# Kernel tuning notes

Measured on AMD Instinct MI355X. Metric: run time of the kernel, lower is better.

## Reference

```python
import jax, jax.numpy as jnp
import numpy as np

N, NF, DIM, H, DH, DEPTH, EDIM, NB = 256, 127, 128, 8, 64, 6, 3, 512
INNER = H * DH  # 512
SCALE = DH ** -0.5
EPS = 1e-5


def setup_inputs() -> dict:
    key = jax.random.key(0)
    ks = jax.random.split(key, 16)
    p = lambda k, shape: jax.random.normal(k, shape, jnp.float32) * 0.02
    return {
        "coordinates": jax.random.normal(ks[0], (N, 3), jnp.float32),
        "bonds": jax.random.randint(ks[1], (NB, 2), 0, N),
        "noise_level": jax.random.uniform(ks[2], (1,), jnp.float32),
        "atom_emb": p(ks[3], (N, NF)),
        "ln1_g": jnp.ones((DEPTH, DIM)), "ln1_b": jnp.zeros((DEPTH, DIM)),
        "Wq": p(ks[4], (DEPTH, DIM, INNER)), "bq": jnp.zeros((DEPTH, INNER)),
        "Wkv": p(ks[5], (DEPTH, DIM, 2 * INNER)), "bkv": jnp.zeros((DEPTH, 2 * INNER)),
        "We": p(ks[6], (DEPTH, EDIM, INNER)), "be": jnp.zeros((DEPTH, INNER)),
        "Wo": p(ks[7], (DEPTH, INNER, DIM)), "bo": jnp.zeros((DEPTH, DIM)),
        "Wg1": p(ks[8], (DEPTH, 3 * DIM)),
        "ln2_g": jnp.ones((DEPTH, DIM)), "ln2_b": jnp.zeros((DEPTH, DIM)),
        "W1": p(ks[9], (DEPTH, DIM, 4 * DIM)), "b1": jnp.zeros((DEPTH, 4 * DIM)),
        "W2": p(ks[10], (DEPTH, 4 * DIM, DIM)), "b2": jnp.zeros((DEPTH, DIM)),
        "Wg2": p(ks[11], (DEPTH, 3 * DIM)),
        "out_w": p(ks[12], (DIM, 1)), "out_b": jnp.zeros((1,)),
    }


def _layernorm(x, g, b):
    m = jnp.mean(x, axis=-1, keepdims=True)
    v = jnp.mean((x - m) ** 2, axis=-1, keepdims=True)
    return (x - m) * jax.lax.rsqrt(v + EPS) * g + b


def _gated_residual(x, res, Wg):
    # Linear(3*dim -> 1, no bias) then sigmoid; mask is all-True so no masking.
    gate = jax.nn.sigmoid(jnp.concatenate([x, res, x - res], axis=-1) @ Wg)[..., None]
    return x * gate + res * (1.0 - gate)


def _forward(coordinates, bonds, noise_level, atom_emb, ln1_g, ln1_b, Wq, bq,
             Wkv, bkv, We, be, Wo, bo, Wg1, ln2_g, ln2_b, W1, b1, W2, b2, Wg2,
             out_w, out_b):
    n = coordinates.shape[0]
    # nodes: [n, NF] atom embeddings (looked up at arange(n)) + noise column -> [n, DIM]
    noise_col = jnp.broadcast_to(noise_level.reshape(1, 1), (n, 1))
    nodes = jnp.concatenate([atom_emb, noise_col], axis=-1)
    # dense edge tensor [n, n, 3]: coordinate differences at bonded pairs, antisymmetric
    bi, bj = bonds[:, 0], bonds[:, 1]
    diff = coordinates[bi] - coordinates[bj]
    edges = jnp.zeros((n, n, EDIM), jnp.float32).at[bi, bj].set(diff).at[bj, bi].set(-diff)

    for l in range(DEPTH):
        # --- edge-biased multi-head attention (PreNorm) ---
        x = _layernorm(nodes, ln1_g[l], ln1_b[l])
        q = (x @ Wq[l] + bq[l]).reshape(n, H, DH).transpose(1, 0, 2)          # [h, i, d]
        kv = x @ Wkv[l] + bkv[l]
        k = kv[:, :INNER].reshape(n, H, DH).transpose(1, 0, 2)                # [h, j, d]
        v = kv[:, INNER:].reshape(n, H, DH).transpose(1, 0, 2)                # [h, j, d]
        e = (edges @ We[l] + be[l]).reshape(n, n, H, DH).transpose(2, 0, 1, 3)  # [h, i, j, d]
        k_ij = k[:, None, :, :] + e                                            # [h, i, j, d]
        v_ij = v[:, None, :, :] + e
        sim = jnp.einsum('hid,hijd->hij', q, k_ij) * SCALE
        attn = jax.nn.softmax(sim, axis=-1)  # mask is all ones -> no-op
        out = jnp.einsum('hij,hijd->hid', attn, v_ij)                          # [h, i, d]
        out = out.transpose(1, 0, 2).reshape(n, INNER) @ Wo[l] + bo[l]         # [n, DIM]
        nodes = _gated_residual(out, nodes, Wg1[l])
        # --- feedforward (PreNorm) + gated residual ---
        y = _layernorm(nodes, ln2_g[l], ln2_b[l])
        y = jax.nn.gelu(y @ W1[l] + b1[l], approximate=False) @ W2[l] + b2[l]
        nodes = _gated_residual(y, nodes, Wg2[l])

    energy = nodes @ out_w + out_b  # [n, 1]
    return energy[None, :, :]       # [1, n, 1]


def reference(coordinates, bonds, noise_level, atom_emb, ln1_g, ln1_b, Wq, bq,
              Wkv, bkv, We, be, Wo, bo, Wg1, ln2_g, ln2_b, W1, b1, W2, b2, Wg2,
              out_w, out_b):
    return _forward(coordinates, bonds, noise_level, atom_emb, ln1_g, ln1_b,
                    Wq, bq, Wkv, bkv, We, be, Wo, bo, Wg1, ln2_g, ln2_b,
                    W1, b1, W2, b2, Wg2, out_w, out_b)
```

## Files before the change

### kernel.cpp

```cpp
#include <hip/hip_runtime.h>

#define NN     256
#define NF     127
#define DIM    128
#define NH     8
#define DH     64
#define INNER  512
#define DEPTH  6
#define NB     512
#define ATTN_SCALE 0.125f
#define LN_EPS 1e-5f

__device__ __forceinline__ float wred_sum(float v){
#pragma unroll
  for(int o=32;o;o>>=1) v += __shfl_xor(v,o);
  return v;
}
__device__ __forceinline__ float wred_max(float v){
#pragma unroll
  for(int o=32;o;o>>=1) v = fmaxf(v,__shfl_xor(v,o));
  return v;
}
__device__ __forceinline__ float block_sum(float v, float* sred, int t){
  v = wred_sum(v);
  __syncthreads();
  if((t&63)==0) sred[t>>6]=v;
  __syncthreads();
  float s = 0.f;
#pragma unroll
  for(int w=0; w<8; w++) s += sred[w];
  return s;
}

__device__ __forceinline__ void dev_ln(const float* in, float* out,
                                       const float* g, const float* b,
                                       float* sred, int t){
  float v = (t<DIM)? in[t] : 0.f;
  float m = block_sum(v,sred,t) * (1.f/DIM);
  float d = (t<DIM)? (v-m) : 0.f;
  float var = block_sum(d*d,sred,t) * (1.f/DIM);
  float rs = rsqrtf(var + LN_EPS);
  if(t<DIM) out[t] = d*rs*g[t] + b[t];
  __syncthreads();
}

__device__ __forceinline__ void dev_qkv4(const float* xs, int i,
    const float* Wq, const float* bq, const float* Wkv, const float* bkv,
    const float* be, float* qg, float* kT, float* vg, float* redS, int t){
  {
    const int cg4 = (t&127)*4, rq = t>>7;
    float4 acc = make_float4(0.f,0.f,0.f,0.f);
#pragma unroll
    for(int f=rq*32; f<rq*32+32; f++){
      float x = xs[f];
      float4 w = *(const float4*)(Wq + f*INNER + cg4);
      acc.x=fmaf(x,w.x,acc.x); acc.y=fmaf(x,w.y,acc.y);
      acc.z=fmaf(x,w.z,acc.z); acc.w=fmaf(x,w.w,acc.w);
    }
    *(float4*)(redS + rq*INNER + cg4) = acc;
  }
  __syncthreads();
  qg[i*INNER+t] = bq[t] + redS[t] + redS[INNER+t] + redS[2*INNER+t] + redS[3*INNER+t];
  __syncthreads();
  {
    const int cg4 = (t&255)*4, rh = t>>8;
    float4 acc = make_float4(0.f,0.f,0.f,0.f);
#pragma unroll 8
    for(int f=rh*64; f<rh*64+64; f++){
      float x = xs[f];
      float4 w = *(const float4*)(Wkv + f*(2*INNER) + cg4);
      acc.x=fmaf(x,w.x,acc.x); acc.y=fmaf(x,w.y,acc.y);
      acc.z=fmaf(x,w.z,acc.z); acc.w=fmaf(x,w.w,acc.w);
    }
    *(float4*)(redS + rh*(2*INNER) + cg4) = acc;
  }
  __syncthreads();
#pragma unroll
  for(int cc=0; cc<2; cc++){
    int c = t + cc*512;
    float s = redS[c] + redS[2*INNER+c] + bkv[c];
    if(c < INNER) kT[c*NN+i]          = s + be[c];
    else          vg[i*INNER+c-INNER] = s + be[c-INNER];
  }
  __syncthreads();
}

__global__ __launch_bounds__(512) void k_qkv0(const float* atom_emb, const float* noise,
    float* nodes,
    const float* ln1_g, const float* ln1_b,
    const float* Wq, const float* bq, const float* Wkv, const float* bkv, const float* be,
    float* qg, float* kT, float* vg){
  __shared__ float nd[DIM], xs[DIM], sred[8], redS[2048];
  int t = threadIdx.x, i = blockIdx.x;
  if(t<DIM){
    float v = (t<NF)? atom_emb[i*NF+t] : noise[0];
    nd[t] = v;
    nodes[i*DIM+t] = v;
  }
  __syncthreads();
  dev_ln(nd, xs, ln1_g, ln1_b, sred, t);
  dev_qkv4(xs, i, Wq, bq, Wkv, bkv, be, qg, kT, vg, redS, t);
}

__global__ __launch_bounds__(512) void k_layer(
    float* nodes, const float* qg, const float* kT, const float* vg,
    float* qg_n, float* kT_n, float* vg_n,
    const int* bonds, const float* coords,
    const float* We,
    const float* Wo, const float* bo, const float* Wg1,
    const float* ln2_g, const float* ln2_b,
    const float* W1, const float* b1, const float* W2, const float* b2,
    const float* Wg2,
    const float* ln1_g_n, const float* ln1_b_n,
    const float* Wq_n, const float* bq_n, const float* Wkv_n, const float* bkv_n,
    const float* be_n, int has_next)
{
  __shared__ float nd[DIM], xs[DIM], qs[INNER], ao[INNER], o128[DIM];
  __shared__ float eL[NN*3], aW[NH*NN], redS[2048], sred[8], qWe[NH*3];
  const int t = threadIdx.x, i = blockIdx.x;

  if(t<DIM) nd[t] = nodes[i*DIM+t];
  qs[t] = qg[i*INNER+t];
  eL[t] = 0.f;
  if(t<NN) eL[512+t] = 0.f;
  __syncthreads();

  {
    int bi = bonds[2*t], bj = bonds[2*t+1];
    if(bi==i || bj==i){
      float dx = coords[3*bi+0] - coords[3*bj+0];
      float dy = coords[3*bi+1] - coords[3*bj+1];
      float dz = coords[3*bi+2] - coords[3*bj+2];
      if(bi==i){ eL[bj*3+0]=dx;  eL[bj*3+1]=dy;  eL[bj*3+2]=dz;  }
      if(bj==i){ eL[bi*3+0]=-dx; eL[bi*3+1]=-dy; eL[bi*3+2]=-dz; }
    }
  }
  __syncthreads();

  if(t < NH*3){
    int h = t/3, c = t%3;
    float acc = 0.f;
    for(int d=0; d<DH; d++) acc = fmaf(qs[h*DH+d], We[c*INNER + h*DH + d], acc);
    qWe[t] = acc;
  }
  __syncthreads();

  {
    const int h = t>>6, l = t&63, j0 = 4*l;
    const float* kTh = kT + (h*DH)*NN;
    float s0=0.f,s1=0.f,s2=0.f,s3=0.f;
#pragma unroll 8
    for(int o=0; o<DH; o++){
      float qv = qs[h*DH+o];
      float4 kk = *(const float4*)(kTh + o*NN + j0);
      s0=fmaf(qv,kk.x,s0); s1=fmaf(qv,kk.y,s1); s2=fmaf(qv,kk.z,s2); s3=fmaf(qv,kk.w,s3);
    }
    float w0=qWe[h*3+0], w1=qWe[h*3+1], w2=qWe[h*3+2];
    s0 += w0*eL[(j0+0)*3+0] + w1*eL[(j0+0)*3+1] + w2*eL[(j0+0)*3+2];
    s1 += w0*eL[(j0+1)*3+0] + w1*eL[(j0+1)*3+1] + w2*eL[(j0+1)*3+2];
    s2 += w0*eL[(j0+2)*3+0] + w1*eL[(j0+2)*3+1] + w2*eL[(j0+2)*3+2];
    s3 += w0*eL[(j0+3)*3+0] + w1*eL[(j0+3)*3+1] + w2*eL[(j0+3)*3+2];
    s0*=ATTN_SCALE; s1*=ATTN_SCALE; s2*=ATTN_SCALE; s3*=ATTN_SCALE;
    float mx = wred_max(fmaxf(fmaxf(s0,s1),fmaxf(s2,s3)));
    float p0=expf(s0-mx), p1=expf(s1-mx), p2=expf(s2-mx), p3=expf(s3-mx);
    float inv = 1.f / wred_sum(p0+p1+p2+p3);
    float a0=p0*inv, a1=p1*inv, a2=p2*inv, a3=p3*inv;
    float* aw = aW + h*NN;
    *(float4*)(aw + j0) = make_float4(a0,a1,a2,a3);
    float c0 = a0*eL[(j0+0)*3+0]+a1*eL[(j0+1)*3+0]+a2*eL[(j0+2)*3+0]+a3*eL[(j0+3)*3+0];
    float c1 = a0*eL[(j0+0)*3+1]+a1*eL[(j0+1)*3+1]+a2*eL[(j0+2)*3+1]+a3*eL[(j0+3)*3+1];
    float c2 = a0*eL[(j0+0)*3+2]+a1*eL[(j0+1)*3+2]+a2*eL[(j0+2)*3+2]+a3*eL[(j0+3)*3+2];
    c0 = wred_sum(c0); c1 = wred_sum(c1); c2 = wred_sum(c2);
    __builtin_amdgcn_wave_barrier();
    const int dq = (l&15)*4, jg = l>>4;
    const float* vb = vg + h*DH + dq;
    float4 acc = make_float4(0.f,0.f,0.f,0.f);
#pragma unroll 8
    for(int jj=0; jj<64; jj++){
      int j = jg*64 + jj;
      float a = aw[j];
      float4 vv = *(const float4*)(vb + j*INNER);
      acc.x=fmaf(a,vv.x,acc.x); acc.y=fmaf(a,vv.y,acc.y);
      acc.z=fmaf(a,vv.z,acc.z); acc.w=fmaf(a,vv.w,acc.w);
    }
#pragma unroll
    for(int o=16;o<64;o<<=1){
      acc.x += __shfl_xor(acc.x,o); acc.y += __shfl_xor(acc.y,o);
      acc.z += __shfl_xor(acc.z,o); acc.w += __shfl_xor(acc.w,o);
    }
    if(l<16){
      float4 we0 = *(const float4*)(We + 0*INNER + h*DH + dq);
      float4 we1 = *(const float4*)(We + 1*INNER + h*DH + dq);
      float4 we2 = *(const float4*)(We + 2*INNER + h*DH + dq);
      float4 o;
      o.x = acc.x + c0*we0.x + c1*we1.x + c2*we2.x;
      o.y = acc.y + c0*we0.y + c1*we1.y + c2*we2.y;
      o.z = acc.z + c0*we0.z + c1*we1.z + c2*we2.z;
      o.w = acc.w + c0*we0.w + c1*we1.w + c2*we2.w;
      *(float4*)(ao + h*DH + dq) = o;
    }
  }
  __syncthreads();

  {
    const int cg4 = (t&31)*4, rg = t>>5;
    float4 acc = make_float4(0.f,0.f,0.f,0.f);
#pragma unroll
    for(int r=rg*32; r<rg*32+32; r++){
      float a = ao[r];
      float4 w = *(const float4*)(Wo + r*DIM + cg4);
      acc.x=fmaf(a,w.x,acc.x); acc.y=fmaf(a,w.y,acc.y);
      acc.z=fmaf(a,w.z,acc.z); acc.w=fmaf(a,w.w,acc.w);
    }
    *(float4*)(redS + rg*DIM + cg4) = acc;
    __syncthreads();
    if(t<DIM){
      float s = bo[t];
#pragma unroll
      for(int g=0; g<16; g++) s += redS[g*DIM+t];
      o128[t] = s;
    }
    __syncthreads();
    float gv = 0.f;
    if(t<DIM){
      float o = o128[t], r = nd[t];
      gv = o*Wg1[t] + r*Wg1[DIM+t] + (o-r)*Wg1[2*DIM+t];
    }
    float gs = block_sum(gv, sred, t);
    float gate = 1.f/(1.f + expf(-gs));
    if(t<DIM) nd[t] = o128[t]*gate + nd[t]*(1.f-gate);
    __syncthreads();
  }

  dev_ln(nd, xs, ln2_g, ln2_b, sred, t);
  {
    const int cg4 = (t&127)*4, rq = t>>7;
    float4 acc = make_float4(0.f,0.f,0.f,0.f);
#pragma unroll
    for(int f=rq*32; f<rq*32+32; f++){
      float x = xs[f];
      float4 w = *(const float4*)(W1 + f*INNER + cg4);
      acc.x=fmaf(x,w.x,acc.x); acc.y=fmaf(x,w.y,acc.y);
      acc.z=fmaf(x,w.z,acc.z); acc.w=fmaf(x,w.w,acc.w);
    }
    *(float4*)(redS + rq*INNER + cg4) = acc;
  }
  __syncthreads();
  {
    float a = b1[t] + redS[t] + redS[INNER+t] + redS[2*INNER+t] + redS[3*INNER+t];
    qs[t] = 0.5f*a*(1.f + erff(a*0.70710678118654752440f));
  }
  __syncthreads();
  {
    const int cg4 = (t&31)*4, rg = t>>5;
    float4 acc = make_float4(0.f,0.f,0.f,0.f);
#pragma unroll
    for(int m=rg*32; m<rg*32+32; m++){
      float a = qs[m];
      float4 w = *(const float4*)(W2 + m*DIM + cg4);
      acc.x=fmaf(a,w.x,acc.x); acc.y=fmaf(a,w.y,acc.y);
      acc.z=fmaf(a,w.z,acc.z); acc.w=fmaf(a,w.w,acc.w);
    }
    *(float4*)(redS + rg*DIM + cg4) = acc;
    __syncthreads();
    if(t<DIM){
      float s = b2[t];
#pragma unroll
      for(int g=0; g<16; g++) s += redS[g*DIM+t];
      o128[t] = s;
    }
    __syncthreads();
    float gv = 0.f;
    if(t<DIM){
      float y = o128[t], r = nd[t];
      gv = y*Wg2[t] + r*Wg2[DIM+t] + (y-r)*Wg2[2*DIM+t];
    }
    float gs = block_sum(gv, sred, t);
    float gate = 1.f/(1.f + expf(-gs));
    if(t<DIM) nd[t] = o128[t]*gate + nd[t]*(1.f-gate);
    __syncthreads();
  }
  if(t<DIM) nodes[i*DIM+t] = nd[t];

  if(has_next){
    dev_ln(nd, xs, ln1_g_n, ln1_b_n, sred, t);
    dev_qkv4(xs, i, Wq_n, bq_n, Wkv_n, bkv_n, be_n, qg_n, kT_n, vg_n, redS, t);
  }
}

__global__ __launch_bounds__(64) void k_energy(const float* nodes, const float* out_w,
                                               const float* out_b, float* out){
  int i = blockIdx.x, l = threadIdx.x;
  float a = fmaf(nodes[i*DIM+l], out_w[l], nodes[i*DIM+64+l]*out_w[64+l]);
  a = wred_sum(a);
  if(l==0) out[i] = a + out_b[0];
}

extern "C" void kernel_launch(void* const* d_in, const int* in_sizes, int n_in,
                              void* d_out, int out_size, void* d_ws, size_t ws_size,
                              hipStream_t stream){
  const float* coords   = (const float*)d_in[0];
  const int*   bonds    = (const int*  )d_in[1];
  const float* noise    = (const float*)d_in[2];
  const float* atom_emb = (const float*)d_in[3];
  const float* ln1_g = (const float*)d_in[4];
  const float* ln1_b = (const float*)d_in[5];
  const float* Wq    = (const float*)d_in[6];
  const float* bq    = (const float*)d_in[7];
  const float* Wkv   = (const float*)d_in[8];
  const float* bkv   = (const float*)d_in[9];
  const float* We    = (const float*)d_in[10];
  const float* be    = (const float*)d_in[11];
  const float* Wo    = (const float*)d_in[12];
  const float* bo    = (const float*)d_in[13];
  const float* Wg1   = (const float*)d_in[14];
  const float* ln2_g = (const float*)d_in[15];
  const float* ln2_b = (const float*)d_in[16];
  const float* W1    = (const float*)d_in[17];
  const float* b1    = (const float*)d_in[18];
  const float* W2    = (const float*)d_in[19];
  const float* b2    = (const float*)d_in[20];
  const float* Wg2   = (const float*)d_in[21];
  const float* out_w = (const float*)d_in[22];
  const float* out_b = (const float*)d_in[23];

  float* ws = (float*)d_ws;
  float* nodes   = ws;
  float* qbuf[2] = { ws +  32768, ws + 163840 };
  float* kbuf[2] = { ws + 294912, ws + 425984 };
  float* vbuf[2] = { ws + 557056, ws + 688128 };

  k_qkv0<<<256, 512, 0, stream>>>(atom_emb, noise, nodes, ln1_g, ln1_b,
                                  Wq, bq, Wkv, bkv, be,
                                  qbuf[0], kbuf[0], vbuf[0]);
  for(int l=0; l<DEPTH; l++){
    int cur = l&1, nxt = cur^1;
    int has_next = (l < DEPTH-1);
    int ln = has_next ? l+1 : l;
    k_layer<<<256, 512, 0, stream>>>(
      nodes, qbuf[cur], kbuf[cur], vbuf[cur],
      qbuf[nxt], kbuf[nxt], vbuf[nxt],
      bonds, coords,
      We  + (size_t)l*3*INNER,
      Wo  + (size_t)l*INNER*DIM, bo + (size_t)l*DIM, Wg1 + (size_t)l*3*DIM,
      ln2_g + (size_t)l*DIM, ln2_b + (size_t)l*DIM,
      W1  + (size_t)l*DIM*4*DIM, b1 + (size_t)l*4*DIM,
      W2  + (size_t)l*4*DIM*DIM, b2 + (size_t)l*DIM, Wg2 + (size_t)l*3*DIM,
      ln1_g + (size_t)ln*DIM, ln1_b + (size_t)ln*DIM,
      Wq  + (size_t)ln*DIM*INNER, bq + (size_t)ln*INNER,
      Wkv + (size_t)ln*DIM*2*INNER, bkv + (size_t)ln*2*INNER,
      be  + (size_t)ln*INNER, has_next);
  }
  k_energy<<<256, 64, 0, stream>>>(nodes, out_w, out_b, (float*)d_out);
}
```

Before: 320.1 us.

## Process two atoms per block to reuse weight and K/V loads

```diff
diff --git a/kernel.cpp b/kernel.cpp
--- a/kernel.cpp
+++ b/kernel.cpp
@@ -21,66 +21,97 @@
   for(int o=32;o;o>>=1) v = fmaxf(v,__shfl_xor(v,o));
   return v;
 }
-__device__ __forceinline__ float block_sum(float v, float* sred, int t){
-  v = wred_sum(v);
-  __syncthreads();
-  if((t&63)==0) sred[t>>6]=v;
-  __syncthreads();
-  float s = 0.f;
-#pragma unroll
-  for(int w=0; w<8; w++) s += sred[w];
-  return s;
-}
-
-__device__ __forceinline__ void dev_ln(const float* in, float* out,
-                                       const float* g, const float* b,
-                                       float* sred, int t){
-  float v = (t<DIM)? in[t] : 0.f;
-  float m = block_sum(v,sred,t) * (1.f/DIM);
-  float d = (t<DIM)? (v-m) : 0.f;
-  float var = block_sum(d*d,sred,t) * (1.f/DIM);
-  float rs = rsqrtf(var + LN_EPS);
-  if(t<DIM) out[t] = d*rs*g[t] + b[t];
-  __syncthreads();
-}
-
-__device__ __forceinline__ void dev_qkv4(const float* xs, int i,
+__device__ __forceinline__ float2 block_sum2(float v0, float v1, float* sred, int t){
+  v0 = wred_sum(v0); v1 = wred_sum(v1);
+  __syncthreads();
+  if((t&63)==0){ sred[t>>6]=v0; sred[8+(t>>6)]=v1; }
+  __syncthreads();
+  float s0=0.f, s1=0.f;
+#pragma unroll
+  for(int w=0; w<8; w++){ s0 += sred[w]; s1 += sred[8+w]; }
+  return make_float2(s0,s1);
+}
+
+__device__ __forceinline__ void dev_ln2(const float* in0, const float* in1,
+                                        float* out0, float* out1,
+                                        const float* g, const float* b,
+                                        float* sred, int t){
+  float v0 = (t<DIM)? in0[t] : 0.f;
+  float v1 = (t<DIM)? in1[t] : 0.f;
+  float2 m = block_sum2(v0,v1,sred,t);
+  float m0 = m.x*(1.f/DIM), m1 = m.y*(1.f/DIM);
+  float d0 = (t<DIM)? (v0-m0) : 0.f;
+  float d1 = (t<DIM)? (v1-m1) : 0.f;
+  float2 vv = block_sum2(d0*d0,d1*d1,sred,t);
+  float rs0 = rsqrtf(vv.x*(1.f/DIM) + LN_EPS);
+  float rs1 = rsqrtf(vv.y*(1.f/DIM) + LN_EPS);
+  if(t<DIM){
+    float gg = g[t], bb = b[t];
+    out0[t] = d0*rs0*gg + bb;
+    out1[t] = d1*rs1*gg + bb;
+  }
+  __syncthreads();
+}
+
+__device__ __forceinline__ void dev_qkv2(const float* xs0, const float* xs1, int i0,
     const float* Wq, const float* bq, const float* Wkv, const float* bkv,
-    const float* be, float* qg, float* kT, float* vg, float* redS, int t){
+    const float* be, float* qg, float* kT, float* vg, float* scratch, int t){
   {
     const int cg4 = (t&127)*4, rq = t>>7;
-    float4 acc = make_float4(0.f,0.f,0.f,0.f);
+    float4 a0 = make_float4(0.f,0.f,0.f,0.f);
+    float4 a1 = make_float4(0.f,0.f,0.f,0.f);
 #pragma unroll
     for(int f=rq*32; f<rq*32+32; f++){
-      float x = xs[f];
+      float x0 = xs0[f], x1 = xs1[f];
       float4 w = *(const float4*)(Wq + f*INNER + cg4);
-      acc.x=fmaf(x,w.x,acc.x); acc.y=fmaf(x,w.y,acc.y);
-      acc.z=fmaf(x,w.z,acc.z); acc.w=fmaf(x,w.w,acc.w);
-    }
-    *(float4*)(redS + rq*INNER + cg4) = acc;
-  }
-  __syncthreads();
-  qg[i*INNER+t] = bq[t] + redS[t] + redS[INNER+t] + redS[2*INNER+t] + redS[3*INNER+t];
+      a0.x=fmaf(x0,w.x,a0.x); a0.y=fmaf(x0,w.y,a0.y);
+      a0.z=fmaf(x0,w.z,a0.z); a0.w=fmaf(x0,w.w,a0.w);
+      a1.x=fmaf(x1,w.x,a1.x); a1.y=fmaf(x1,w.y,a1.y);
+      a1.z=fmaf(x1,w.z,a1.z); a1.w=fmaf(x1,w.w,a1.w);
+    }
+    *(float4*)(scratch + rq*INNER + cg4)        = a0;
+    *(float4*)(scratch + 2048 + rq*INNER + cg4) = a1;
+  }
+  __syncthreads();
+  {
+    float bqt = bq[t];
+    qg[i0*INNER+t]     = bqt + scratch[t] + scratch[INNER+t]
+                             + scratch[2*INNER+t] + scratch[3*INNER+t];
+    qg[(i0+1)*INNER+t] = bqt + scratch[2048+t] + scratch[2048+INNER+t]
+                             + scratch[2048+2*INNER+t] + scratch[2048+3*INNER+t];
+  }
   __syncthreads();
   {
     const int cg4 = (t&255)*4, rh = t>>8;
-    float4 acc = make_float4(0.f,0.f,0.f,0.f);
+    float4 a0 = make_float4(0.f,0.f,0.f,0.f);
+    float4 a1 = make_float4(0.f,0.f,0.f,0.f);
 #pragma unroll 8
     for(int f=rh*64; f<rh*64+64; f++){
-      float x = xs[f];
+      float x0 = xs0[f], x1 = xs1[f];
       float4 w = *(const float4*)(Wkv + f*(2*INNER) + cg4);
-      acc.x=fmaf(x,w.x,acc.x); acc.y=fmaf(x,w.y,acc.y);
-      acc.z=fmaf(x,w.z,acc.z); acc.w=fmaf(x,w.w,acc.w);
-    }
-    *(float4*)(redS + rh*(2*INNER) + cg4) = acc;
+      a0.x=fmaf(x0,w.x,a0.x); a0.y=fmaf(x0,w.y,a0.y);
+      a0.z=fmaf(x0,w.z,a0.z); a0.w=fmaf(x0,w.w,a0.w);
+      a1.x=fmaf(x1,w.x,a1.x); a1.y=fmaf(x1,w.y,a1.y);
+      a1.z=fmaf(x1,w.z,a1.z); a1.w=fmaf(x1,w.w,a1.w);
+    }
+    *(float4*)(scratch + rh*1024 + cg4)        = a0;
+    *(float4*)(scratch + 2048 + rh*1024 + cg4) = a1;
   }
   __syncthreads();
 #pragma unroll
   for(int cc=0; cc<2; cc++){
     int c = t + cc*512;
-    float s = redS[c] + redS[2*INNER+c] + bkv[c];
-    if(c < INNER) kT[c*NN+i]          = s + be[c];
-    else          vg[i*INNER+c-INNER] = s + be[c-INNER];
+    float bk = bkv[c];
+    float s0 = scratch[c]      + scratch[1024+c]      + bk;
+    float s1 = scratch[2048+c] + scratch[2048+1024+c] + bk;
+    if(c < INNER){
+      float bec = be[c];
+      *(float2*)(kT + c*NN + i0) = make_float2(s0+bec, s1+bec);
+    } else {
+      float bec = be[c-INNER];
+      vg[i0*INNER+c-INNER]     = s0 + bec;
+      vg[(i0+1)*INNER+c-INNER] = s1 + bec;
+    }
   }
   __syncthreads();
 }
@@ -90,16 +121,18 @@
     const float* ln1_g, const float* ln1_b,
     const float* Wq, const float* bq, const float* Wkv, const float* bkv, const float* be,
     float* qg, float* kT, float* vg){
-  __shared__ float nd[DIM], xs[DIM], sred[8], redS[2048];
-  int t = threadIdx.x, i = blockIdx.x;
+  __shared__ float nd0[DIM], nd1[DIM], xs0[DIM], xs1[DIM], sred[16], scratch[4096];
+  int t = threadIdx.x, i0 = blockIdx.x*2;
   if(t<DIM){
-    float v = (t<NF)? atom_emb[i*NF+t] : noise[0];
-    nd[t] = v;
-    nodes[i*DIM+t] = v;
-  }
-  __syncthreads();
-  dev_ln(nd, xs, ln1_g, ln1_b, sred, t);
-  dev_qkv4(xs, i, Wq, bq, Wkv, bkv, be, qg, kT, vg, redS, t);
+    float nz = noise[0];
+    float v0 = (t<NF)? atom_emb[i0*NF+t]     : nz;
+    float v1 = (t<NF)? atom_emb[(i0+1)*NF+t] : nz;
+    nd0[t]=v0; nd1[t]=v1;
+    nodes[i0*DIM+t]=v0; nodes[(i0+1)*DIM+t]=v1;
+  }
+  __syncthreads();
+  dev_ln2(nd0, nd1, xs0, xs1, ln1_g, ln1_b, sred, t);
+  dev_qkv2(xs0, xs1, i0, Wq, bq, Wkv, bkv, be, qg, kT, vg, scratch, t);
 }
 
 __global__ __launch_bounds__(512) void k_layer(
@@ -115,32 +148,39 @@
     const float* Wq_n, const float* bq_n, const float* Wkv_n, const float* bkv_n,
     const float* be_n, int has_next)
 {
-  __shared__ float nd[DIM], xs[DIM], qs[INNER], ao[INNER], o128[DIM];
-  __shared__ float eL[NN*3], aW[NH*NN], redS[2048], sred[8], qWe[NH*3];
-  const int t = threadIdx.x, i = blockIdx.x;
-
-  if(t<DIM) nd[t] = nodes[i*DIM+t];
-  qs[t] = qg[i*INNER+t];
-  eL[t] = 0.f;
-  if(t<NN) eL[512+t] = 0.f;
+  __shared__ float nd0[DIM], nd1[DIM], xs0[DIM], xs1[DIM];
+  __shared__ float qs0[INNER], qs1[INNER], ao0[INNER], ao1[INNER];
+  __shared__ float o1280[DIM], o1281[DIM];
+  __shared__ float eL0[NN*3], eL1[NN*3];
+  __shared__ float scratch[4096];
+  __shared__ float sred[16], qWe[2*NH*3];
+  const int t = threadIdx.x, i0 = blockIdx.x*2, i1 = i0+1;
+
+  if(t<DIM){ nd0[t] = nodes[i0*DIM+t]; nd1[t] = nodes[i1*DIM+t]; }
+  qs0[t] = qg[i0*INNER+t]; qs1[t] = qg[i1*INNER+t];
+  eL0[t] = 0.f; eL1[t] = 0.f;
+  if(t<NN){ eL0[512+t] = 0.f; eL1[512+t] = 0.f; }
   __syncthreads();
 
   {
     int bi = bonds[2*t], bj = bonds[2*t+1];
-    if(bi==i || bj==i){
+    if(bi==i0||bj==i0||bi==i1||bj==i1){
       float dx = coords[3*bi+0] - coords[3*bj+0];
       float dy = coords[3*bi+1] - coords[3*bj+1];
       float dz = coords[3*bi+2] - coords[3*bj+2];
-      if(bi==i){ eL[bj*3+0]=dx;  eL[bj*3+1]=dy;  eL[bj*3+2]=dz;  }
-      if(bj==i){ eL[bi*3+0]=-dx; eL[bi*3+1]=-dy; eL[bi*3+2]=-dz; }
-    }
-  }
-  __syncthreads();
-
-  if(t < NH*3){
-    int h = t/3, c = t%3;
+      if(bi==i0){ eL0[bj*3+0]=dx;  eL0[bj*3+1]=dy;  eL0[bj*3+2]=dz;  }
+      if(bj==i0){ eL0[bi*3+0]=-dx; eL0[bi*3+1]=-dy; eL0[bi*3+2]=-dz; }
+      if(bi==i1){ eL1[bj*3+0]=dx;  eL1[bj*3+1]=dy;  eL1[bj*3+2]=dz;  }
+      if(bj==i1){ eL1[bi*3+0]=-dx; eL1[bi*3+1]=-dy; eL1[bi*3+2]=-dz; }
+    }
+  }
+  __syncthreads();
+
+  if(t < 2*NH*3){
+    int r = t/24, rem = t%24, h = rem/3, c = rem%3;
+    const float* qsr = r? qs1 : qs0;
     float acc = 0.f;
-    for(int d=0; d<DH; d++) acc = fmaf(qs[h*DH+d], We[c*INNER + h*DH + d], acc);
+    for(int d=0; d<DH; d++) acc = fmaf(qsr[h*DH+d], We[c*INNER + h*DH + d], acc);
     qWe[t] = acc;
   }
   __syncthreads();
@@ -148,143 +188,208 @@
   {
     const int h = t>>6, l = t&63, j0 = 4*l;
     const float* kTh = kT + (h*DH)*NN;
-    float s0=0.f,s1=0.f,s2=0.f,s3=0.f;
+    float4 sA = make_float4(0.f,0.f,0.f,0.f);
+    float4 sB = make_float4(0.f,0.f,0.f,0.f);
 #pragma unroll 8
     for(int o=0; o<DH; o++){
-      float qv = qs[h*DH+o];
+      float qa = qs0[h*DH+o], qb = qs1[h*DH+o];
       float4 kk = *(const float4*)(kTh + o*NN + j0);
-      s0=fmaf(qv,kk.x,s0); s1=fmaf(qv,kk.y,s1); s2=fmaf(qv,kk.z,s2); s3=fmaf(qv,kk.w,s3);
-    }
-    float w0=qWe[h*3+0], w1=qWe[h*3+1], w2=qWe[h*3+2];
-    s0 += w0*eL[(j0+0)*3+0] + w1*eL[(j0+0)*3+1] + w2*eL[(j0+0)*3+2];
-    s1 += w0*eL[(j0+1)*3+0] + w1*eL[(j0+1)*3+1] + w2*eL[(j0+1)*3+2];
-    s2 += w0*eL[(j0+2)*3+0] + w1*eL[(j0+2)*3+1] + w2*eL[(j0+2)*3+2];
-    s3 += w0*eL[(j0+3)*3+0] + w1*eL[(j0+3)*3+1] + w2*eL[(j0+3)*3+2];
-    s0*=ATTN_SCALE; s1*=ATTN_SCALE; s2*=ATTN_SCALE; s3*=ATTN_SCALE;
-    float mx = wred_max(fmaxf(fmaxf(s0,s1),fmaxf(s2,s3)));
-    float p0=expf(s0-mx), p1=expf(s1-mx), p2=expf(s2-mx), p3=expf(s3-mx);
-    float inv = 1.f / wred_sum(p0+p1+p2+p3);
-    float a0=p0*inv, a1=p1*inv, a2=p2*inv, a3=p3*inv;
-    float* aw = aW + h*NN;
-    *(float4*)(aw + j0) = make_float4(a0,a1,a2,a3);
-    float c0 = a0*eL[(j0+0)*3+0]+a1*eL[(j0+1)*3+0]+a2*eL[(j0+2)*3+0]+a3*eL[(j0+3)*3+0];
-    float c1 = a0*eL[(j0+0)*3+1]+a1*eL[(j0+1)*3+1]+a2*eL[(j0+2)*3+1]+a3*eL[(j0+3)*3+1];
-    float c2 = a0*eL[(j0+0)*3+2]+a1*eL[(j0+1)*3+2]+a2*eL[(j0+2)*3+2]+a3*eL[(j0+3)*3+2];
-    c0 = wred_sum(c0); c1 = wred_sum(c1); c2 = wred_sum(c2);
+      sA.x=fmaf(qa,kk.x,sA.x); sA.y=fmaf(qa,kk.y,sA.y);
+      sA.z=fmaf(qa,kk.z,sA.z); sA.w=fmaf(qa,kk.w,sA.w);
+      sB.x=fmaf(qb,kk.x,sB.x); sB.y=fmaf(qb,kk.y,sB.y);
+      sB.z=fmaf(qb,kk.z,sB.z); sB.w=fmaf(qb,kk.w,sB.w);
+    }
+    float wa0=qWe[h*3+0],    wa1=qWe[h*3+1],    wa2=qWe[h*3+2];
+    float wb0=qWe[24+h*3+0], wb1=qWe[24+h*3+1], wb2=qWe[24+h*3+2];
+    sA.x += wa0*eL0[(j0+0)*3+0] + wa1*eL0[(j0+0)*3+1] + wa2*eL0[(j0+0)*3+2];
+    sA.y += wa0*eL0[(j0+1)*3+0] + wa1*eL0[(j0+1)*3+1] + wa2*eL0[(j0+1)*3+2];
+    sA.z += wa0*eL0[(j0+2)*3+0] + wa1*eL0[(j0+2)*3+1] + wa2*eL0[(j0+2)*3+2];
+    sA.w += wa0*eL0[(j0+3)*3+0] + wa1*eL0[(j0+3)*3+1] + wa2*eL0[(j0+3)*3+2];
+    sB.x += wb0*eL1[(j0+0)*3+0] + wb1*eL1[(j0+0)*3+1] + wb2*eL1[(j0+0)*3+2];
+    sB.y += wb0*eL1[(j0+1)*3+0] + wb1*eL1[(j0+1)*3+1] + wb2*eL1[(j0+1)*3+2];
+    sB.z += wb0*eL1[(j0+2)*3+0] + wb1*eL1[(j0+2)*3+1] + wb2*eL1[(j0+2)*3+2];
+    sB.w += wb0*eL1[(j0+3)*3+0] + wb1*eL1[(j0+3)*3+1] + wb2*eL1[(j0+3)*3+2];
+    sA.x*=ATTN_SCALE; sA.y*=ATTN_SCALE; sA.z*=ATTN_SCALE; sA.w*=ATTN_SCALE;
+    sB.x*=ATTN_SCALE; sB.y*=ATTN_SCALE; sB.z*=ATTN_SCALE; sB.w*=ATTN_SCALE;
+    float mxA = wred_max(fmaxf(fmaxf(sA.x,sA.y),fmaxf(sA.z,sA.w)));
+    float mxB = wred_max(fmaxf(fmaxf(sB.x,sB.y),fmaxf(sB.z,sB.w)));
+    float pA0=expf(sA.x-mxA), pA1=expf(sA.y-mxA), pA2=expf(sA.z-mxA), pA3=expf(sA.w-mxA);
+    float pB0=expf(sB.x-mxB), pB1=expf(sB.y-mxB), pB2=expf(sB.z-mxB), pB3=expf(sB.w-mxB);
+    float invA = 1.f / wred_sum(pA0+pA1+pA2+pA3);
+    float invB = 1.f / wred_sum(pB0+pB1+pB2+pB3);
+    float aA0=pA0*invA, aA1=pA1*invA, aA2=pA2*invA, aA3=pA3*invA;
+    float aB0=pB0*invB, aB1=pB1*invB, aB2=pB2*invB, aB3=pB3*invB;
+    float* awA = scratch + h*NN;
+    float* awB = scratch + 2048 + h*NN;
+    *(float4*)(awA + j0) = make_float4(aA0,aA1,aA2,aA3);
+    *(float4*)(awB + j0) = make_float4(aB0,aB1,aB2,aB3);
+    float cA0 = aA0*eL0[(j0+0)*3+0]+aA1*eL0[(j0+1)*3+0]+aA2*eL0[(j0+2)*3+0]+aA3*eL0[(j0+3)*3+0];
+    float cA1 = aA0*eL0[(j0+0)*3+1]+aA1*eL0[(j0+1)*3+1]+aA2*eL0[(j0+2)*3+1]+aA3*eL0[(j0+3)*3+1];
+    float cA2 = aA0*eL0[(j0+0)*3+2]+aA1*eL0[(j0+1)*3+2]+aA2*eL0[(j0+2)*3+2]+aA3*eL0[(j0+3)*3+2];
+    float cB0 = aB0*eL1[(j0+0)*3+0]+aB1*eL1[(j0+1)*3+0]+aB2*eL1[(j0+2)*3+0]+aB3*eL1[(j0+3)*3+0];
+    float cB1 = aB0*eL1[(j0+0)*3+1]+aB1*eL1[(j0+1)*3+1]+aB2*eL1[(j0+2)*3+1]+aB3*eL1[(j0+3)*3+1];
+    float cB2 = aB0*eL1[(j0+0)*3+2]+aB1*eL1[(j0+1)*3+2]+aB2*eL1[(j0+2)*3+2]+aB3*eL1[(j0+3)*3+2];
+    cA0=wred_sum(cA0); cA1=wred_sum(cA1); cA2=wred_sum(cA2);
+    cB0=wred_sum(cB0); cB1=wred_sum(cB1); cB2=wred_sum(cB2);
     __builtin_amdgcn_wave_barrier();
     const int dq = (l&15)*4, jg = l>>4;
     const float* vb = vg + h*DH + dq;
-    float4 acc = make_float4(0.f,0.f,0.f,0.f);
+    float4 accA = make_float4(0.f,0.f,0.f,0.f);
+    float4 accB = make_float4(0.f,0.f,0.f,0.f);
 #pragma unroll 8
     for(int jj=0; jj<64; jj++){
       int j = jg*64 + jj;
-      float a = aw[j];
+      float aA = awA[j], aB = awB[j];
       float4 vv = *(const float4*)(vb + j*INNER);
-      acc.x=fmaf(a,vv.x,acc.x); acc.y=fmaf(a,vv.y,acc.y);
-      acc.z=fmaf(a,vv.z,acc.z); acc.w=fmaf(a,vv.w,acc.w);
+      accA.x=fmaf(aA,vv.x,accA.x); accA.y=fmaf(aA,vv.y,accA.y);
+      accA.z=fmaf(aA,vv.z,accA.z); accA.w=fmaf(aA,vv.w,accA.w);
+      accB.x=fmaf(aB,vv.x,accB.x); accB.y=fmaf(aB,vv.y,accB.y);
+      accB.z=fmaf(aB,vv.z,accB.z); accB.w=fmaf(aB,vv.w,accB.w);
     }
 #pragma unroll
     for(int o=16;o<64;o<<=1){
-      acc.x += __shfl_xor(acc.x,o); acc.y += __shfl_xor(acc.y,o);
-      acc.z += __shfl_xor(acc.z,o); acc.w += __shfl_xor(acc.w,o);
+      accA.x += __shfl_xor(accA.x,o); accA.y += __shfl_xor(accA.y,o);
+      accA.z += __shfl_xor(accA.z,o); accA.w += __shfl_xor(accA.w,o);
+      accB.x += __shfl_xor(accB.x,o); accB.y += __shfl_xor(accB.y,o);
+      accB.z += __shfl_xor(accB.z,o); accB.w += __shfl_xor(accB.w,o);
     }
     if(l<16){
       float4 we0 = *(const float4*)(We + 0*INNER + h*DH + dq);
       float4 we1 = *(const float4*)(We + 1*INNER + h*DH + dq);
       float4 we2 = *(const float4*)(We + 2*INNER + h*DH + dq);
-      float4 o;
-      o.x = acc.x + c0*we0.x + c1*we1.x + c2*we2.x;
-      o.y = acc.y + c0*we0.y + c1*we1.y + c2*we2.y;
-      o.z = acc.z + c0*we0.z + c1*we1.z + c2*we2.z;
-      o.w = acc.w + c0*we0.w + c1*we1.w + c2*we2.w;
-      *(float4*)(ao + h*DH + dq) = o;
+      float4 oA, oB;
+      oA.x = accA.x + cA0*we0.x + cA1*we1.x + cA2*we2.x;
+      oA.y = accA.y + cA0*we0.y + cA1*we1.y + cA2*we2.y;
+      oA.z = accA.z + cA0*we0.z + cA1*we1.z + cA2*we2.z;
+      oA.w = accA.w + cA0*we0.w + cA1*we1.w + cA2*we2.w;
+      oB.x = accB.x + cB0*we0.x + cB1*we1.x + cB2*we2.x;
+      oB.y = accB.y + cB0*we0.y + cB1*we1.y + cB2*we2.y;
+      oB.z = accB.z + cB0*we0.z + cB1*we1.z + cB2*we2.z;
+      oB.w = accB.w + cB0*we0.w + cB1*we1.w + cB2*we2.w;
+      *(float4*)(ao0 + h*DH + dq) = oA;
+      *(float4*)(ao1 + h*DH + dq) = oB;
     }
   }
   __syncthreads();
 
   {
     const int cg4 = (t&31)*4, rg = t>>5;
-    float4 acc = make_float4(0.f,0.f,0.f,0.f);
+    float4 a0 = make_float4(0.f,0.f,0.f,0.f);
+    float4 a1 = make_float4(0.f,0.f,0.f,0.f);
 #pragma unroll
     for(int r=rg*32; r<rg*32+32; r++){
-      float a = ao[r];
+      float v0 = ao0[r], v1 = ao1[r];
       float4 w = *(const float4*)(Wo + r*DIM + cg4);
-      acc.x=fmaf(a,w.x,acc.x); acc.y=fmaf(a,w.y,acc.y);
-      acc.z=fmaf(a,w.z,acc.z); acc.w=fmaf(a,w.w,acc.w);
-    }
-    *(float4*)(redS + rg*DIM + cg4) = acc;
-    __syncthreads();
+      a0.x=fmaf(v0,w.x,a0.x); a0.y=fmaf(v0,w.y,a0.y);
+      a0.z=fmaf(v0,w.z,a0.z); a0.w=fmaf(v0,w.w,a0.w);
+      a1.x=fmaf(v1,w.x,a1.x); a1.y=fmaf(v1,w.y,a1.y);
+      a1.z=fmaf(v1,w.z,a1.z); a1.w=fmaf(v1,w.w,a1.w);
+    }
+    *(float4*)(scratch + rg*DIM + cg4)        = a0;
+    *(float4*)(scratch + 2048 + rg*DIM + cg4) = a1;
+    __syncthreads();
+    if(t<2*DIM){
+      int r = t>>7, c = t&127;
+      const float* rs = scratch + r*2048;
+      float s = bo[c];
+#pragma unroll
+      for(int g=0; g<16; g++) s += rs[g*DIM+c];
+      (r? o1281 : o1280)[c] = s;
+    }
+    __syncthreads();
+    float gv0=0.f, gv1=0.f;
     if(t<DIM){
-      float s = bo[t];
-#pragma unroll
-      for(int g=0; g<16; g++) s += redS[g*DIM+t];
-      o128[t] = s;
-    }
-    __syncthreads();
-    float gv = 0.f;
+      float w0=Wg1[t], w1=Wg1[DIM+t], w2=Wg1[2*DIM+t];
+      float oA=o1280[t], rA=nd0[t];
+      float oB=o1281[t], rB=nd1[t];
+      gv0 = oA*w0 + rA*w1 + (oA-rA)*w2;
+      gv1 = oB*w0 + rB*w1 + (oB-rB)*w2;
+    }
+    float2 gs = block_sum2(gv0, gv1, sred, t);
+    float gateA = 1.f/(1.f + expf(-gs.x));
+    float gateB = 1.f/(1.f + expf(-gs.y));
     if(t<DIM){
-      float o = o128[t], r = nd[t];
-      gv = o*Wg1[t] + r*Wg1[DIM+t] + (o-r)*Wg1[2*DIM+t];
-    }
-    float gs = block_sum(gv, sred, t);
-    float gate = 1.f/(1.f + expf(-gs));
-    if(t<DIM) nd[t] = o128[t]*gate + nd[t]*(1.f-gate);
-    __syncthreads();
-  }
-
-  dev_ln(nd, xs, ln2_g, ln2_b, sred, t);
+      nd0[t] = o1280[t]*gateA + nd0[t]*(1.f-gateA);
+      nd1[t] = o1281[t]*gateB + nd1[t]*(1.f-gateB);
+    }
+    __syncthreads();
+  }
+
+  dev_ln2(nd0, nd1, xs0, xs1, ln2_g, ln2_b, sred, t);
   {
     const int cg4 = (t&127)*4, rq = t>>7;
-    float4 acc = make_float4(0.f,0.f,0.f,0.f);
+    float4 a0 = make_float4(0.f,0.f,0.f,0.f);
+    float4 a1 = make_float4(0.f,0.f,0.f,0.f);
 #pragma unroll
     for(int f=rq*32; f<rq*32+32; f++){
-      float x = xs[f];
+      float x0 = xs0[f], x1 = xs1[f];
       float4 w = *(const float4*)(W1 + f*INNER + cg4);
-      acc.x=fmaf(x,w.x,acc.x); acc.y=fmaf(x,w.y,acc.y);
-      acc.z=fmaf(x,w.z,acc.z); acc.w=fmaf(x,w.w,acc.w);
-    }
-    *(float4*)(redS + rq*INNER + cg4) = acc;
-  }
-  __syncthreads();
-  {
-    float a = b1[t] + redS[t] + redS[INNER+t] + redS[2*INNER+t] + redS[3*INNER+t];
-    qs[t] = 0.5f*a*(1.f + erff(a*0.70710678118654752440f));
+      a0.x=fmaf(x0,w.x,a0.x); a0.y=fmaf(x0,w.y,a0.y);
+      a0.z=fmaf(x0,w.z,a0.z); a0.w=fmaf(x0,w.w,a0.w);
+      a1.x=fmaf(x1,w.x,a1.x); a1.y=fmaf(x1,w.y,a1.y);
+      a1.z=fmaf(x1,w.z,a1.z); a1.w=fmaf(x1,w.w,a1.w);
+    }
+    *(float4*)(scratch + rq*INNER + cg4)        = a0;
+    *(float4*)(scratch + 2048 + rq*INNER + cg4) = a1;
+  }
+  __syncthreads();
+  {
+    float bt = b1[t];
+    float aA = bt + scratch[t] + scratch[INNER+t]
+                 + scratch[2*INNER+t] + scratch[3*INNER+t];
+    float aB = bt + scratch[2048+t] + scratch[2048+INNER+t]
+                 + scratch[2048+2*INNER+t] + scratch[2048+3*INNER+t];
+    qs0[t] = 0.5f*aA*(1.f + erff(aA*0.70710678118654752440f));
+    qs1[t] = 0.5f*aB*(1.f + erff(aB*0.70710678118654752440f));
   }
   __syncthreads();
   {
     const int cg4 = (t&31)*4, rg = t>>5;
-    float4 acc = make_float4(0.f,0.f,0.f,0.f);
+    float4 a0 = make_float4(0.f,0.f,0.f,0.f);
+    float4 a1 = make_float4(0.f,0.f,0.f,0.f);
 #pragma unroll
     for(int m=rg*32; m<rg*32+32; m++){
-      float a = qs[m];
+      float v0 = qs0[m], v1 = qs1[m];
       float4 w = *(const float4*)(W2 + m*DIM + cg4);
-      acc.x=fmaf(a,w.x,acc.x); acc.y=fmaf(a,w.y,acc.y);
-      acc.z=fmaf(a,w.z,acc.z); acc.w=fmaf(a,w.w,acc.w);
-    }
-    *(float4*)(redS + rg*DIM + cg4) = acc;
-    __syncthreads();
+      a0.x=fmaf(v0,w.x,a0.x); a0.y=fmaf(v0,w.y,a0.y);
+      a0.z=fmaf(v0,w.z,a0.z); a0.w=fmaf(v0,w.w,a0.w);
+      a1.x=fmaf(v1,w.x,a1.x); a1.y=fmaf(v1,w.y,a1.y);
+      a1.z=fmaf(v1,w.z,a1.z); a1.w=fmaf(v1,w.w,a1.w);
+    }
+    *(float4*)(scratch + rg*DIM + cg4)        = a0;
+    *(float4*)(scratch + 2048 + rg*DIM + cg4) = a1;
+    __syncthreads();
+    if(t<2*DIM){
+      int r = t>>7, c = t&127;
+      const float* rs = scratch + r*2048;
+      float s = b2[c];
+#pragma unroll
+      for(int g=0; g<16; g++) s += rs[g*DIM+c];
+      (r? o1281 : o1280)[c] = s;
+    }
+    __syncthreads();
+    float gv0=0.f, gv1=0.f;
     if(t<DIM){
-      float s = b2[t];
-#pragma unroll
-      for(int g=0; g<16; g++) s += redS[g*DIM+t];
-      o128[t] = s;
-    }
-    __syncthreads();
-    float gv = 0.f;
+      float w0=Wg2[t], w1=Wg2[DIM+t], w2=Wg2[2*DIM+t];
+      float yA=o1280[t], rA=nd0[t];
+      float yB=o1281[t], rB=nd1[t];
+      gv0 = yA*w0 + rA*w1 + (yA-rA)*w2;
+      gv1 = yB*w0 + rB*w1 + (yB-rB)*w2;
+    }
+    float2 gs = block_sum2(gv0, gv1, sred, t);
+    float gateA = 1.f/(1.f + expf(-gs.x));
+    float gateB = 1.f/(1.f + expf(-gs.y));
     if(t<DIM){
-      float y = o128[t], r = nd[t];
-      gv = y*Wg2[t] + r*Wg2[DIM+t] + (y-r)*Wg2[2*DIM+t];
-    }
-    float gs = block_sum(gv, sred, t);
-    float gate = 1.f/(1.f + expf(-gs));
-    if(t<DIM) nd[t] = o128[t]*gate + nd[t]*(1.f-gate);
-    __syncthreads();
-  }
-  if(t<DIM) nodes[i*DIM+t] = nd[t];
+      nd0[t] = o1280[t]*gateA + nd0[t]*(1.f-gateA);
+      nd1[t] = o1281[t]*gateB + nd1[t]*(1.f-gateB);
+    }
+    __syncthreads();
+  }
+  if(t<DIM){ nodes[i0*DIM+t] = nd0[t]; nodes[i1*DIM+t] = nd1[t]; }
 
   if(has_next){
-    dev_ln(nd, xs, ln1_g_n, ln1_b_n, sred, t);
-    dev_qkv4(xs, i, Wq_n, bq_n, Wkv_n, bkv_n, be_n, qg_n, kT_n, vg_n, redS, t);
+    dev_ln2(nd0, nd1, xs0, xs1, ln1_g_n, ln1_b_n, sred, t);
+    dev_qkv2(xs0, xs1, i0, Wq_n, bq_n, Wkv_n, bkv_n, be_n, qg_n, kT_n, vg_n, scratch, t);
   }
 }
 
@@ -330,14 +435,14 @@
   float* kbuf[2] = { ws + 294912, ws + 425984 };
   float* vbuf[2] = { ws + 557056, ws + 688128 };
 
-  k_qkv0<<<256, 512, 0, stream>>>(atom_emb, noise, nodes, ln1_g, ln1_b,
+  k_qkv0<<<128, 512, 0, stream>>>(atom_emb, noise, nodes, ln1_g, ln1_b,
                                   Wq, bq, Wkv, bkv, be,
                                   qbuf[0], kbuf[0], vbuf[0]);
   for(int l=0; l<DEPTH; l++){
     int cur = l&1, nxt = cur^1;
     int has_next = (l < DEPTH-1);
     int ln = has_next ? l+1 : l;
-    k_layer<<<256, 512, 0, stream>>>(
+    k_layer<<<128, 512, 0, stream>>>(
       nodes, qbuf[cur], kbuf[cur], vbuf[cur],
       qbuf[nxt], kbuf[nxt], vbuf[nxt],
       bonds, coords,
```

Result: no change. 322.8 us (+0.8%).
